# Kernel tuning notes

Measured on AMD Instinct MI355X. Metric: run time of the kernel, lower is better.

## Reference

```python
import jax, jax.numpy as jnp
import numpy as np

KSIZE = 3
SCALE = 2


def setup_inputs() -> dict:
    key = jax.random.key(0)
    k1, k2, k3, k4 = jax.random.split(key, 4)
    B, C, H, W = 8, 3, 512, 512
    h, w = H // SCALE, W // SCALE
    return {
        "images": jax.random.uniform(k1, (B, C, H, W), jnp.float32),
        "kernels": jax.random.uniform(k2, (B, KSIZE ** 2, h, w), jnp.float32),
        "offsets_x": jax.random.uniform(k3, (B, KSIZE ** 2, h, w), jnp.float32),
        "offsets_y": jax.random.uniform(k4, (B, KSIZE ** 2, h, w), jnp.float32),
    }


def _softround(x, alpha=1.0):
    two_pi = 2.0 * jnp.pi
    return x - alpha * (jnp.sin(two_pi * x) / two_pi)


def _batch_bli(im, x, y):
    # im: [B, H, W, 3] channel-last; x, y: [B, N] float coords
    B, N = x.shape
    x0 = jnp.floor(x).astype(jnp.int32)
    x1 = x0 + 1
    y0 = jnp.floor(y).astype(jnp.int32)
    y1 = y0 + 1
    # original clamps x by im.shape[2] and y by im.shape[1] (square images)
    x0 = jnp.clip(x0, 0, im.shape[2] - 1)
    x1 = jnp.clip(x1, 0, im.shape[2] - 1)
    y0 = jnp.clip(y0, 0, im.shape[1] - 1)
    y1 = jnp.clip(y1, 0, im.shape[1] - 1)
    bidx = jnp.arange(B)[:, None]
    # vectorized gather of the four corners; flatten like torch.cat of [3]-vectors
    Ia = im[bidx, x0, y0].reshape(-1)  # [B*N*3]
    Ib = im[bidx, x0, y1].reshape(-1)
    Ic = im[bidx, x1, y0].reshape(-1)
    Id = im[bidx, x1, y1].reshape(-1)
    scale_w = (1.0 / ((x1 - x0) * (y1 - y0))).reshape(-1)  # [B*N]
    # faithful to the original's (scrambling) reshape semantics
    m1 = jnp.concatenate([x1 - x, x - x0], axis=1).astype(jnp.float32)  # [B, 2N]
    m1 = jnp.tile(m1.reshape(B * N, 1, 1, 2), (1, 2, 1, 1))             # [BN,2,1,2]
    m2 = jnp.stack([Ib, Ia, Id, Ic], axis=1).reshape(B * N, 2, 2, 3)    # [BN,2,2,3]
    m3 = jnp.concatenate([y1 - y, y - y0], axis=1).astype(jnp.float32)
    m3 = m3.reshape(B * N, 1, 2, 1)                                     # [BN,1,2,1]
    t = jnp.matmul(m1, m2).transpose(0, 3, 2, 1)  # [BN,3,1,2]
    out = jnp.matmul(t, m3).reshape(B * N, 3)     # [BN,3]
    return scale_w[:, None] * out


def reference(images, kernels, offsets_x, offsets_y):
    B = images.shape[0]
    h, w = images.shape[2] // SCALE, images.shape[3] // SCALE
    kernels = kernels.transpose(0, 2, 3, 1)      # [B,h,w,9]
    ox = offsets_x.transpose(0, 2, 3, 1)         # [B,h,w,9]
    oy = offsets_y.transpose(0, 2, 3, 1)
    u = jnp.arange(h, dtype=jnp.float32) + 0.5 * SCALE - 0.5
    kx = jnp.repeat(jnp.arange(KSIZE), KSIZE).astype(jnp.float32)  # 0,0,0,1,1,1,2,2,2
    ky = jnp.tile(jnp.arange(KSIZE), KSIZE).astype(jnp.float32)    # 0,1,2,0,1,2,0,1,2
    # original broadcasts u.reshape(h,1) over the w axis (requires h == w)
    coords_x = ox + KSIZE / 2 + kx + u[:, None]
    coords_y = oy + KSIZE / 2 + ky + u[:, None]
    im = images.transpose(0, 2, 3, 1)  # [B,H,W,3]
    pix = _batch_bli(im, coords_x.reshape(B, -1), coords_y.reshape(B, -1))
    pix_hr = pix.reshape(B, h, w, KSIZE ** 2, 3)
    out = jnp.sum(kernels[..., None] * pix_hr, axis=-2)  # [B,h,w,3]
    return _softround(out * 255.0)
```

## Files before the change

kernel.cpp:

```cpp
#include <hip/hip_runtime.h>
#include <math.h>

#define BATCH 8
#define HI 512
#define WI 512
#define HO 256
#define WO 256
#define PLANE (HI*WI)
#define OPIX (HO*WO)
#define LROWS 68
#define LCOLS 10
#define LQ 11

__global__ __launch_bounds__(256, 8) void downsampler_kernel(
    const float* __restrict__ images,
    const float* __restrict__ kernels,
    const float* __restrict__ offx,
    const float* __restrict__ offy,
    float* __restrict__ out)
{
    __shared__ float4 simg[LROWS * LQ];

    const int blk  = blockIdx.x;
    const int b    = blk >> 8;
    const int ihx  = (blk >> 2) & 63;
    const int w0   = (blk & 3) << 6;
    const int tid  = threadIdx.x;
    const int lane = tid & 63;
    const int iw   = w0 + lane;
    const int ih   = (ihx << 2) + (tid >> 6);

    {
        const float* imb = images + (size_t)b * 3 * PLANE;
        for (int i = tid; i < LROWS * LCOLS; i += 256) {
            const int row = i / LCOLS;
            const int col = i - row * LCOLS;
            const int r = w0 + 2 + row;
            int c = r - 4 + col;
            c = c < 0 ? 0 : c;
            const float* src = imb + r * WI + c;
            simg[row * LQ + col] =
                make_float4(src[0], src[PLANE], src[2 * PLANE], 0.0f);
        }
    }
    __syncthreads();

    const bool flip = (ih < 128);
    const float* offxb = offx    + (size_t)b * 9 * OPIX;
    const float* offyb = offy    + (size_t)b * 9 * OPIX;
    const float* kernb = kernels + (size_t)b * 9 * OPIX;

    const int pl   = ih * WO + iw;
    const int pix2 = pl & (OPIX / 2 - 1);

    const float uu_own = (float)iw + 0.5f;
    const float uu_s0  = (float)((2 * iw) & 255) + 0.5f;
    const float uu_s1  = uu_s0 + 1.0f;

    float acc0 = 0.f, acc1 = 0.f, acc2 = 0.f;

    #pragma unroll
    for (int k = 0; k < 9; ++k) {
        const float oxv = offxb[k * OPIX + pl];
        const float oyv = offyb[k * OPIX + pl];
        const float kvv = kernb[k * OPIX + pl];
        const int ta = 2 * k, tb = 2 * k + 1;
        const int sel_a = (ta >= 9) ? 1 : 0;
        const int sel_b = (tb >= 9) ? 1 : 0;
        const int ks_a = ta - 9 * sel_a;
        const int ks_b = tb - 9 * sel_b;
        const float2 sxa = ((const float2*)(offxb + ks_a * OPIX))[pix2];
        const float2 sya = ((const float2*)(offyb + ks_a * OPIX))[pix2];
        const float2 sxb = ((const float2*)(offxb + ks_b * OPIX))[pix2];
        const float2 syb = ((const float2*)(offyb + ks_b * OPIX))[pix2];

        const float kxf = (float)(k / 3);
        const float kyf = (float)(k - 3 * (k / 3));
        const float cx = ((oxv + 1.5f) + kxf) + uu_own;
        const float cy = ((oyv + 1.5f) + kyf) + uu_own;
        const int x0 = (int)floorf(cx);
        const int y0 = (int)floorf(cy);
        const int rowrel = x0 - 2 - w0;
        const int colq   = y0 - x0 + 4;
        const float4* qa = &simg[rowrel * LQ + (colq - 1)];
        const float4 Ia = qa[1];
        const float4 Ib = qa[2];
        const float4 Ic = qa[LQ];
        const float4 Id = qa[LQ + 1];

        const float uu_a = sel_a ? uu_s1 : uu_s0;
        const float uu_b = sel_b ? uu_s1 : uu_s0;
        const float oxa  = sel_a ? sxa.y : sxa.x;
        const float oya  = sel_a ? sya.y : sya.x;
        const float oxb2 = sel_b ? sxb.y : sxb.x;
        const float oyb2 = sel_b ? syb.y : syb.x;
        const float kxa = (float)(ks_a / 3), kya = (float)(ks_a - 3 * (ks_a / 3));
        const float kxb = (float)(ks_b / 3), kyb = (float)(ks_b - 3 * (ks_b / 3));

        const float cxa = ((oxa + 1.5f) + kxa) + uu_a;
        const float cya = ((oya + 1.5f) + kya) + uu_a;
        const float cxb = ((oxb2 + 1.5f) + kxb) + uu_b;
        const float cyb = ((oyb2 + 1.5f) + kyb) + uu_b;
        const float fxa = cxa - floorf(cxa);
        const float fya = cya - floorf(cya);
        const float fxb = cxb - floorf(cxb);
        const float fyb = cyb - floorf(cyb);
        const float w0w = flip ? (1.0f - fxa) : fxa;
        const float w1w = flip ? (1.0f - fxb) : fxb;
        const float v0w = flip ? (1.0f - fya) : fya;
        const float v1w = flip ? (1.0f - fyb) : fyb;

        const float w0v0 = w0w * v0w, w1v0 = w1w * v0w;
        const float w0v1 = w0w * v1w, w1v1 = w1w * v1w;

        const float p0 = w0v0 * Ib.x + w1v0 * Ic.x + w0v1 * Id.y + w1v1 * Ia.z;
        const float p1 = w0v0 * Ia.x + w1v0 * Ib.y + w0v1 * Ic.y + w1v1 * Id.z;
        const float p2 = w0v0 * Id.x + w1v0 * Ia.y + w0v1 * Ib.z + w1v1 * Ic.z;

        acc0 += kvv * p0;
        acc1 += kvv * p1;
        acc2 += kvv * p2;
    }

    const float TWO_PI_INV = 0.15915494309189533577f;
    const size_t obase = ((size_t)b * OPIX + (size_t)pl) * 3;
    const float z0 = acc0 * 255.0f;
    const float z1 = acc1 * 255.0f;
    const float z2 = acc2 * 255.0f;
    const float r0s = z0 - rintf(z0);
    const float r1s = z1 - rintf(z1);
    const float r2s = z2 - rintf(z2);
    out[obase + 0] = z0 - __builtin_amdgcn_sinf(r0s) * TWO_PI_INV;
    out[obase + 1] = z1 - __builtin_amdgcn_sinf(r1s) * TWO_PI_INV;
    out[obase + 2] = z2 - __builtin_amdgcn_sinf(r2s) * TWO_PI_INV;
}

extern "C" void kernel_launch(void* const* d_in, const int* in_sizes, int n_in,
                              void* d_out, int out_size, void* d_ws, size_t ws_size,
                              hipStream_t stream) {
    const float* images  = (const float*)d_in[0];
    const float* kernels = (const float*)d_in[1];
    const float* offx    = (const float*)d_in[2];
    const float* offy    = (const float*)d_in[3];
    float* out = (float*)d_out;

    dim3 grid(BATCH * 64 * 4);
    dim3 block(256);
    hipLaunchKernelGGL(downsampler_kernel, grid, block, 0, stream,
                       images, kernels, offx, offy, out);
}
```

Measured before the change: 125.3 us.

## Split 9-tap loop across three wavefronts and reduce partial sums in LDS

```diff
diff --git a/kernel.cpp b/kernel.cpp
--- a/kernel.cpp
+++ b/kernel.cpp
@@ -12,7 +12,7 @@
 #define LCOLS 10
 #define LQ 11
 
-__global__ __launch_bounds__(256, 8) void downsampler_kernel(
+__global__ __launch_bounds__(384) void downsampler_kernel(
     const float* __restrict__ images,
     const float* __restrict__ kernels,
     const float* __restrict__ offx,
@@ -20,19 +20,24 @@
     float* __restrict__ out)
 {
     __shared__ float4 simg[LROWS * LQ];
+    __shared__ float  pbuf[2 * 3 * 64 * 3];
 
     const int blk  = blockIdx.x;
-    const int b    = blk >> 8;
-    const int ihx  = (blk >> 2) & 63;
+    const int b    = blk >> 9;
+    const int ihx  = (blk >> 2) & 127;
     const int w0   = (blk & 3) << 6;
     const int tid  = threadIdx.x;
     const int lane = tid & 63;
+    const int grp  = __builtin_amdgcn_readfirstlane(tid >> 6);
+    const int g    = grp % 3;
+    const int rsel = grp / 3;
+    const int ih0  = ihx << 1;
+    const int ih   = ih0 + rsel;
     const int iw   = w0 + lane;
-    const int ih   = (ihx << 2) + (tid >> 6);
 
     {
         const float* imb = images + (size_t)b * 3 * PLANE;
-        for (int i = tid; i < LROWS * LCOLS; i += 256) {
+        for (int i = tid; i < LROWS * LCOLS; i += 384) {
             const int row = i / LCOLS;
             const int col = i - row * LCOLS;
             const int r = w0 + 2 + row;
@@ -45,22 +50,22 @@
     }
     __syncthreads();
 
-    const bool flip = (ih < 128);
+    const bool flip = (ih0 < 128);
     const float* offxb = offx    + (size_t)b * 9 * OPIX;
     const float* offyb = offy    + (size_t)b * 9 * OPIX;
     const float* kernb = kernels + (size_t)b * 9 * OPIX;
 
     const int pl   = ih * WO + iw;
     const int pix2 = pl & (OPIX / 2 - 1);
-
     const float uu_own = (float)iw + 0.5f;
     const float uu_s0  = (float)((2 * iw) & 255) + 0.5f;
     const float uu_s1  = uu_s0 + 1.0f;
 
-    float acc0 = 0.f, acc1 = 0.f, acc2 = 0.f;
+    float a0 = 0.f, a1 = 0.f, a2 = 0.f;
 
     #pragma unroll
-    for (int k = 0; k < 9; ++k) {
+    for (int j = 0; j < 3; ++j) {
+        const int k = 3 * g + j;
         const float oxv = offxb[k * OPIX + pl];
         const float oyv = offyb[k * OPIX + pl];
         const float kvv = kernb[k * OPIX + pl];
@@ -74,8 +79,8 @@
         const float2 sxb = ((const float2*)(offxb + ks_b * OPIX))[pix2];
         const float2 syb = ((const float2*)(offyb + ks_b * OPIX))[pix2];
 
-        const float kxf = (float)(k / 3);
-        const float kyf = (float)(k - 3 * (k / 3));
+        const float kxf = (float)g;
+        const float kyf = (float)j;
         const float cx = ((oxv + 1.5f) + kxf) + uu_own;
         const float cy = ((oyv + 1.5f) + kyf) + uu_own;
         const int x0 = (int)floorf(cx);
@@ -117,22 +122,31 @@
         const float p1 = w0v0 * Ia.x + w1v0 * Ib.y + w0v1 * Ic.y + w1v1 * Id.z;
         const float p2 = w0v0 * Id.x + w1v0 * Ia.y + w0v1 * Ib.z + w1v1 * Ic.z;
 
-        acc0 += kvv * p0;
-        acc1 += kvv * p1;
-        acc2 += kvv * p2;
+        a0 += kvv * p0;
+        a1 += kvv * p1;
+        a2 += kvv * p2;
     }
 
-    const float TWO_PI_INV = 0.15915494309189533577f;
-    const size_t obase = ((size_t)b * OPIX + (size_t)pl) * 3;
-    const float z0 = acc0 * 255.0f;
-    const float z1 = acc1 * 255.0f;
-    const float z2 = acc2 * 255.0f;
-    const float r0s = z0 - rintf(z0);
-    const float r1s = z1 - rintf(z1);
-    const float r2s = z2 - rintf(z2);
-    out[obase + 0] = z0 - __builtin_amdgcn_sinf(r0s) * TWO_PI_INV;
-    out[obase + 1] = z1 - __builtin_amdgcn_sinf(r1s) * TWO_PI_INV;
-    out[obase + 2] = z2 - __builtin_amdgcn_sinf(r2s) * TWO_PI_INV;
+    {
+        const int pb = (grp * 64 + lane) * 3;
+        pbuf[pb + 0] = a0;
+        pbuf[pb + 1] = a1;
+        pbuf[pb + 2] = a2;
+    }
+    __syncthreads();
+
+    {
+        const int r   = tid / 192;
+        const int idx = tid - r * 192;
+        const float s = pbuf[r * 576 + idx]
+                      + pbuf[r * 576 + 192 + idx]
+                      + pbuf[r * 576 + 384 + idx];
+        const float z  = s * 255.0f;
+        const float rs = z - rintf(z);
+        const float TWO_PI_INV = 0.15915494309189533577f;
+        out[((size_t)b * OPIX + (size_t)(ih0 + r) * WO + w0) * 3 + idx] =
+            z - __builtin_amdgcn_sinf(rs) * TWO_PI_INV;
+    }
 }
 
 extern "C" void kernel_launch(void* const* d_in, const int* in_sizes, int n_in,
@@ -144,8 +158,8 @@
     const float* offy    = (const float*)d_in[3];
     float* out = (float*)d_out;
 
-    dim3 grid(BATCH * 64 * 4);
-    dim3 block(256);
+    dim3 grid(BATCH * 128 * 4);
+    dim3 block(384);
     hipLaunchKernelGGL(downsampler_kernel, grid, block, 0, stream,
                        images, kernels, offx, offy, out);
 }
```

Result: faster. 118.3 us (-5.6%).
